# Kernel optimization log

Measured on AMD Instinct MI355X. Metric: run time of the kernel, lower is better.

The kernel has to match this reference:

```python
import jax, jax.numpy as jnp
import numpy as np

N = 100000      # nodes
E = 3200000     # edges (avg degree 32)
F_IN = 512
HID = 256
CLS = 64


def _linear_init(k, fan_in, fan_out):
    lim = 1.0 / np.sqrt(fan_in)
    kw, kb = jax.random.split(k)
    W = jax.random.uniform(kw, (fan_in, fan_out), jnp.float32, -lim, lim)
    b = jax.random.uniform(kb, (fan_out,), jnp.float32, -lim, lim)
    return W, b


def setup_inputs() -> dict:
    key = jax.random.key(0)
    ks = jax.random.split(key, 8)
    x = jax.random.normal(ks[0], (N, F_IN), jnp.float32)
    edge_src = jax.random.randint(ks[1], (E,), 0, N, jnp.int32)
    off = jax.random.randint(ks[2], (E,), 1, N, jnp.int32)
    edge_dst = ((edge_src + off) % N).astype(jnp.int32)  # no self loops
    Wm0, bm0 = _linear_init(ks[3], F_IN, HID)
    Wv0, bv0 = _linear_init(ks[4], F_IN, HID)
    Wm1, bm1 = _linear_init(ks[5], HID, CLS)
    Wv1, bv1 = _linear_init(ks[6], HID, CLS)
    sample = jax.random.normal(ks[7], (N, CLS), jnp.float32)
    return dict(x=x, Wm0=Wm0, bm0=bm0, Wv0=Wv0, bv0=bv0,
                Wm1=Wm1, bm1=bm1, Wv1=Wv1, bv1=bv1,
                sample=sample, edge_src=edge_src, edge_dst=edge_dst)


def reference(x, Wm0, bm0, Wv0, bv0, Wm1, bm1, Wv1, bv1, sample, edge_src, edge_dst):
    n = x.shape[0]
    loops = jnp.arange(n, dtype=edge_src.dtype)
    src = jnp.concatenate([edge_src, loops])  # fill_diag(adj, 1.0)
    dst = jnp.concatenate([edge_dst, loops])
    ones = jnp.ones(src.shape[0], x.dtype)
    deg = jax.ops.segment_sum(ones, src, num_segments=n)
    dis = jnp.where(deg > 0, deg ** -0.5, 0.0)   # D^-0.5
    di = jnp.where(deg > 0, 1.0 / deg, 0.0)      # D^-1
    w0 = dis[src] * dis[dst]                      # adj0 = D^-0.5 A D^-0.5
    w1 = di[src] * di[dst]                        # adj1 = D^-1  A D^-1

    def spmm(w, m):  # (adj @ m) with edge weights w
        return jax.ops.segment_sum(w[:, None] * m[dst], src, num_segments=n)

    # layer 0 (initial=True): no aggregation, dropout off (eval)
    mean = jax.nn.elu(x @ Wm0 + bm0)
    var = jax.nn.relu(x @ Wv0 + bv0)
    # layer 1: variance-attention + dual SpMM
    mean = jax.nn.elu(mean @ Wm1 + bm1)
    var = jax.nn.relu(var @ Wv1 + bv1) + 1e-6
    attn = jnp.exp(-var)
    mean = spmm(w0, mean * attn)
    var = spmm(w1, var * attn * attn)

    out = mean + sample * jnp.sqrt(var)
    return jax.nn.log_softmax(out, axis=-1)
```

## Files before the change

### kernel.cpp

```cpp
#include <hip/hip_runtime.h>
#include <cstdint>
#include <cstddef>


typedef _Float16 h8 __attribute__((ext_vector_type(8)));
typedef _Float16 h2 __attribute__((ext_vector_type(2)));
typedef float f32x4 __attribute__((ext_vector_type(4)));
typedef unsigned int uint32;

#define BSHIFT 7
#define NCHUNK 256

static __device__ __forceinline__ float elu_f(float z) {
  return z > 0.f ? z : expm1f(z);
}

static __device__ __forceinline__ void gload16(const void* g, void* l) {
  __builtin_amdgcn_global_load_lds(
      (__attribute__((address_space(1))) void*)g,
      (__attribute__((address_space(3))) void*)l, 16, 0, 0);
}

__global__ __launch_bounds__(256) void hist_k(const int* __restrict__ esrc, int E,
                                              int chunk, int* __restrict__ h, int NB) {
  __shared__ int sh[1024];
  int t = threadIdx.x;
  for (int i = t; i < NB; i += 256) sh[i] = 0;
  __syncthreads();
  int e0 = blockIdx.x * chunk;
  int e1 = min(e0 + chunk, E);
  for (int e = e0 + t; e < e1; e += 256) atomicAdd(&sh[esrc[e] >> BSHIFT], 1);
  __syncthreads();
  for (int i = t; i < NB; i += 256) h[blockIdx.x * NB + i] = sh[i];
}

__global__ __launch_bounds__(256) void btotal_k(const int* __restrict__ h,
                                                int* __restrict__ tot, int NB) {
  int b = blockIdx.x, t = threadIdx.x;
  int v = h[t * NB + b];
#pragma unroll
  for (int off = 32; off; off >>= 1) v += __shfl_xor(v, off, 64);
  __shared__ int sw[4];
  if ((t & 63) == 0) sw[t >> 6] = v;
  __syncthreads();
  if (t == 0) tot[b] = sw[0] + sw[1] + sw[2] + sw[3];
}

__global__ __launch_bounds__(1024) void bscan_k(const int* __restrict__ tot,
                                                int* __restrict__ base, int NB) {
  __shared__ int sh[1024];
  int t = threadIdx.x;
  int v = (t < NB) ? tot[t] : 0;
  sh[t] = v;
  __syncthreads();
  for (int off = 1; off < 1024; off <<= 1) {
    int add = (t >= off) ? sh[t - off] : 0;
    __syncthreads();
    sh[t] += add;
    __syncthreads();
  }
  if (t < NB) base[t] = sh[t] - v;
  if (t == 1023) base[NB] = sh[1023];
}

__global__ __launch_bounds__(256) void boff_k(int* __restrict__ h,
                                              const int* __restrict__ base, int NB) {
  __shared__ int sh[256];
  int b = blockIdx.x, t = threadIdx.x;
  int v = h[t * NB + b];
  sh[t] = v;
  __syncthreads();
  for (int off = 1; off < 256; off <<= 1) {
    int add = (t >= off) ? sh[t - off] : 0;
    __syncthreads();
    sh[t] += add;
    __syncthreads();
  }
  h[t * NB + b] = base[b] + sh[t] - v;
}

__global__ __launch_bounds__(256) void bscatter_k(
    const int* __restrict__ esrc, const int* __restrict__ edst, int E, int chunk,
    const int* __restrict__ h, int2* __restrict__ pairs, int NB) {
  __shared__ int lcur[1024];
  int t = threadIdx.x;
  for (int i = t; i < NB; i += 256) lcur[i] = h[blockIdx.x * NB + i];
  __syncthreads();
  int e0 = blockIdx.x * chunk;
  int e1 = min(e0 + chunk, E);
  for (int e = e0 + t; e < e1; e += 256) {
    int s = esrc[e], d = edst[e];
    int pos = atomicAdd(&lcur[s >> BSHIFT], 1);
    pairs[pos] = make_int2(s, d);
  }
}

__global__ __launch_bounds__(256) void countN_k(
    const int2* __restrict__ pairs, const int* __restrict__ base,
    int* __restrict__ cnt, float2* __restrict__ dd, int n) {
  __shared__ int c128[128];
  int b = blockIdx.x, t = threadIdx.x;
  if (t < 128) c128[t] = 0;
  __syncthreads();
  int lo = base[b], hi = base[b + 1];
  for (int i = lo + t; i < hi; i += 256) atomicAdd(&c128[pairs[i].x & 127], 1);
  __syncthreads();
  if (t < 128) {
    int node = b * 128 + t;
    if (node < n) {
      int c = c128[t];
      cnt[node] = c;
      float d = (float)(c + 1);
      dd[node] = make_float2(rsqrtf(d), 1.f / d);
    }
  }
}

__global__ __launch_bounds__(256) void partC_k(
    const int2* __restrict__ pairs, const int* __restrict__ base,
    const int* __restrict__ rs, int* __restrict__ csr, int n) {
  __shared__ int lcur[128];
  int b = blockIdx.x, t = threadIdx.x;
  if (t < 128) {
    int node = b * 128 + t;
    lcur[t] = (node < n) ? rs[node] : 0;
  }
  __syncthreads();
  int lo = base[b], hi = base[b + 1];
  for (int i = lo + t; i < hi; i += 256) {
    int2 pr = pairs[i];
    int pos = atomicAdd(&lcur[pr.x & 127], 1);
    csr[pos] = pr.y;
  }
}

__global__ void scan1_k(const int* __restrict__ cnt, int* __restrict__ excl,
                        int* __restrict__ bsum, int n) {
  __shared__ int sh[256];
  int t = threadIdx.x, idx = blockIdx.x * 256 + t;
  int v = (idx < n) ? ((cnt[idx] + 3) & ~3) : 0;
  sh[t] = v;
  __syncthreads();
  for (int off = 1; off < 256; off <<= 1) {
    int add = (t >= off) ? sh[t - off] : 0;
    __syncthreads();
    sh[t] += add;
    __syncthreads();
  }
  if (idx < n) excl[idx] = sh[t] - v;
  if (t == 255) bsum[blockIdx.x] = sh[255];
}

__global__ void scan2_k(const int* __restrict__ bsum, int* __restrict__ boff, int nb) {
  __shared__ int sh[512];
  int t = threadIdx.x;
  int v = (t < nb) ? bsum[t] : 0;
  sh[t] = v;
  __syncthreads();
  for (int off = 1; off < 512; off <<= 1) {
    int add = (t >= off) ? sh[t - off] : 0;
    __syncthreads();
    sh[t] += add;
    __syncthreads();
  }
  if (t < nb) boff[t] = sh[t] - v;
}

__global__ void scan3_k(int* __restrict__ excl, const int* __restrict__ boff, int n) {
  int idx = blockIdx.x * 256 + threadIdx.x;
  if (idx < n) excl[idx] += boff[blockIdx.x];
}

__global__ void prep_w_k(const float* __restrict__ Wm0, const float* __restrict__ Wv0,
                         const float* __restrict__ Wm1, const float* __restrict__ Wv1,
                         _Float16* __restrict__ W1t, _Float16* __restrict__ W2t) {
  int idx = blockIdx.x * 256 + threadIdx.x;
  if (idx < 512 * 512) {
    int n = idx >> 9, k = idx & 511;
    float v = (n < 256) ? Wm0[k * 256 + n] : Wv0[k * 256 + (n - 256)];
    W1t[idx] = (_Float16)v;
  }
  if (idx < 128 * 512) {
    int n = idx >> 9, k = idx & 511;
    float v = 0.f;
    if (n < 64) { if (k < 256) v = Wm1[k * 64 + n]; }
    else        { if (k >= 256) v = Wv1[(k - 256) * 64 + (n - 64)]; }
    W2t[idx] = (_Float16)v;
  }
}

__global__ __launch_bounds__(512, 2) void gemm1_k(
    const float* __restrict__ A, const _Float16* __restrict__ Bt,
    const float* __restrict__ b0, const float* __restrict__ b1,
    _Float16* __restrict__ out, int M) {
  __shared__ __align__(16) unsigned char ldsb[98304];

  const int m0 = blockIdx.x * 128;
  const int t = threadIdx.x;
  const int lane = t & 63;
  const int wave = t >> 6;
  const int wm = wave >> 2;
  const int wn = wave & 3;
  const int lr = lane & 15, quad = lane >> 4;

  const int ra = t >> 3;
  const int sa = t & 7;
  const int asw = (sa ^ (ra & 7)) << 2;
  const int rb = t >> 2;
  const int sb = t & 3;
  const int bsw = (sb ^ (rb & 3)) << 3;

  f32x4 acc[4][8] = {};

  auto stage = [&](int b, int kt) {
#pragma unroll
    for (int i = 0; i < 2; i++) {
      int r = i * 64 + ra;
      const float* src = A + (size_t)min(m0 + r, M - 1) * 512 + kt + asw;
      gload16(src, ldsb + b * 16384 + i * 8192 + t * 16);
    }
#pragma unroll
    for (int i = 0; i < 4; i++) {
      int r = i * 128 + rb;
      const _Float16* src = Bt + (size_t)r * 512 + kt + bsw;
      gload16(src, ldsb + 32768 + b * 32768 + i * 8192 + t * 16);
    }
  };

  stage(0, 0);
  __syncthreads();

  int cur = 0;
  const int zA = lr & 7;
  const int zB = lr & 3;
  for (int kt = 0; kt < 512; kt += 32) {
    if (kt + 32 < 512) stage(cur ^ 1, kt + 32);
    const unsigned char* Ab = ldsb + cur * 16384;
    const unsigned char* Bb = ldsb + 32768 + cur * 32768;
    h8 bf[8];
#pragma unroll
    for (int j = 0; j < 8; j++) {
      int row = wn * 128 + j * 16 + lr;
      bf[j] = *(const h8*)(Bb + row * 64 + ((quad ^ zB) << 4));
    }
#pragma unroll
    for (int i = 0; i < 4; i++) {
      int R = wm * 64 + i * 16 + lr;
      const float4 a0 = *(const float4*)(Ab + R * 128 + (((2 * quad) ^ zA) << 4));
      const float4 a1 = *(const float4*)(Ab + R * 128 + (((2 * quad + 1) ^ zA) << 4));
      h8 af = {(_Float16)a0.x, (_Float16)a0.y, (_Float16)a0.z, (_Float16)a0.w,
               (_Float16)a1.x, (_Float16)a1.y, (_Float16)a1.z, (_Float16)a1.w};
#pragma unroll
      for (int j = 0; j < 8; j++)
        acc[i][j] = __builtin_amdgcn_mfma_f32_16x16x32_f16(af, bf[j], acc[i][j], 0, 0, 0);
    }
    __syncthreads();
    cur ^= 1;
  }

  _Float16* lt = (_Float16*)ldsb;
  for (int hh = 0; hh < 2; hh++) {
    if (wm == hh) {
#pragma unroll
      for (int j = 0; j < 8; j++) {
        int col = wn * 128 + j * 16 + lr;
        float bj = (col < 256) ? b0[col] : b1[col - 256];
#pragma unroll
        for (int i = 0; i < 4; i++) {
#pragma unroll
          for (int r = 0; r < 4; r++) {
            float z = acc[i][j][r] + bj;
            float v = (col < 256) ? elu_f(z) : fmaxf(z, 0.f);
            lt[(i * 16 + quad * 4 + r) * 520 + col] = (_Float16)v;
          }
        }
      }
    }
    __syncthreads();
    {
      int row = t >> 3;
      int gr = m0 + hh * 64 + row;
      if (gr < M) {
        _Float16* dst = out + (size_t)gr * 512;
        const _Float16* srow = lt + row * 520;
#pragma unroll
        for (int k = 0; k < 8; k++) {
          int c0 = ((t & 7) + k * 8) * 8;
          *(h8*)(dst + c0) = *(const h8*)(srow + c0);
        }
      }
    }
    __syncthreads();
  }
}

__global__ __launch_bounds__(256) void gemm2_k(
    const _Float16* __restrict__ A, const _Float16* __restrict__ Bt,
    const float* __restrict__ bm1, const float* __restrict__ bv1,
    uint32* __restrict__ Mcat, int M, int K) {
  __shared__ _Float16 lds[20480];
  _Float16* As = lds;
  _Float16* Bs = lds + 10240;
  const int m0 = blockIdx.x * 128;
  const int t = threadIdx.x;
  const int lane = t & 63;
  const int wave = t >> 6;
  const int lr = lane & 15, quad = lane >> 4;
  const int trow = t >> 2;
  const int tkc = (t & 3) * 8;

  const size_t arow0 = (size_t)min(m0 + trow, M - 1) * K;
  const size_t arow1 = (size_t)min(m0 + trow + 64, M - 1) * K;
  const size_t brow0 = (size_t)trow * K;
  const size_t brow1 = (size_t)(trow + 64) * K;

  f32x4 acc[2][8] = {};
  h8 pa[2], pb[2];

  pa[0] = *(const h8*)(A + arow0 + tkc);
  pa[1] = *(const h8*)(A + arow1 + tkc);
  pb[0] = *(const h8*)(Bt + brow0 + tkc);
  pb[1] = *(const h8*)(Bt + brow1 + tkc);
  *(h8*)&As[trow * 40 + tkc] = pa[0];
  *(h8*)&As[(trow + 64) * 40 + tkc] = pa[1];
  *(h8*)&Bs[trow * 40 + tkc] = pb[0];
  *(h8*)&Bs[(trow + 64) * 40 + tkc] = pb[1];
  __syncthreads();

  for (int kt = 0; kt < K; kt += 32) {
    const int cur = (kt >> 5) & 1;
    const int curo = cur * 5120;
    const bool more = (kt + 32) < K;
    if (more) {
      pa[0] = *(const h8*)(A + arow0 + kt + 32 + tkc);
      pa[1] = *(const h8*)(A + arow1 + kt + 32 + tkc);
      pb[0] = *(const h8*)(Bt + brow0 + kt + 32 + tkc);
      pb[1] = *(const h8*)(Bt + brow1 + kt + 32 + tkc);
    }
    h8 af[2], bf[8];
#pragma unroll
    for (int i = 0; i < 2; i++)
      af[i] = *(h8*)&As[curo + (wave * 32 + i * 16 + lr) * 40 + quad * 8];
#pragma unroll
    for (int j = 0; j < 8; j++)
      bf[j] = *(h8*)&Bs[curo + (j * 16 + lr) * 40 + quad * 8];
#pragma unroll
    for (int i = 0; i < 2; i++)
#pragma unroll
      for (int j = 0; j < 8; j++)
        acc[i][j] = __builtin_amdgcn_mfma_f32_16x16x32_f16(af[i], bf[j], acc[i][j], 0, 0, 0);
    if (more) {
      const int nxto = (cur ^ 1) * 5120;
      *(h8*)&As[nxto + trow * 40 + tkc] = pa[0];
      *(h8*)&As[nxto + (trow + 64) * 40 + tkc] = pa[1];
      *(h8*)&Bs[nxto + trow * 40 + tkc] = pb[0];
      *(h8*)&Bs[nxto + (trow + 64) * 40 + tkc] = pb[1];
      __syncthreads();
    }
  }

#pragma unroll
  for (int jm = 0; jm < 4; jm++) {
    int c = jm * 16 + lr;
    float bm = bm1[c], bv = bv1[c];
#pragma unroll
    for (int i = 0; i < 2; i++) {
#pragma unroll
      for (int r = 0; r < 4; r++) {
        int gr = m0 + wave * 32 + i * 16 + quad * 4 + r;
        if (gr < M) {
          float zm = acc[i][jm][r] + bm;
          float zv = acc[i][4 + jm][r] + bv;
          float m = elu_f(zm);
          float v = fmaxf(zv, 0.f) + 1e-6f;
          float a = __expf(-v);
          h2 pk;
          pk.x = (_Float16)(m * a);
          pk.y = (_Float16)(v * a * a);
          Mcat[(size_t)gr * 64 + c] = __builtin_bit_cast(uint32, pk);
        }
      }
    }
  }
}

__global__ __launch_bounds__(256) void spmm_final_k(
    const uint32* __restrict__ Mcat, const float2* __restrict__ dd,
    const int* __restrict__ row_start, const int* __restrict__ cnt,
    const int* __restrict__ csr, const float* __restrict__ sample,
    float* __restrict__ out, int n) {
  int wid = threadIdx.x >> 6, lane = threadIdx.x & 63;
  int r = blockIdx.x * 4 + wid;
  if (r >= n) return;
  float2 wr = dd[r];
  h2 self = __builtin_bit_cast(h2, Mcat[(size_t)r * 64 + lane]);
  float Sm = wr.x * (float)self.x;
  float Sv = wr.y * (float)self.y;
  int start = __builtin_amdgcn_readfirstlane(row_start[r]);
  int c = __builtin_amdgcn_readfirstlane(cnt[r]);
  int j = 0;
  for (; j + 4 <= c; j += 4) {
    int4 d4 = *(const int4*)(csr + start + j);
    float2 w0 = dd[d4.x];
    float2 w1 = dd[d4.y];
    float2 w2 = dd[d4.z];
    float2 w3 = dd[d4.w];
    h2 p0 = __builtin_bit_cast(h2, Mcat[(size_t)d4.x * 64 + lane]);
    h2 p1 = __builtin_bit_cast(h2, Mcat[(size_t)d4.y * 64 + lane]);
    h2 p2 = __builtin_bit_cast(h2, Mcat[(size_t)d4.z * 64 + lane]);
    h2 p3 = __builtin_bit_cast(h2, Mcat[(size_t)d4.w * 64 + lane]);
    Sm += w0.x * (float)p0.x; Sv += w0.y * (float)p0.y;
    Sm += w1.x * (float)p1.x; Sv += w1.y * (float)p1.y;
    Sm += w2.x * (float)p2.x; Sv += w2.y * (float)p2.y;
    Sm += w3.x * (float)p3.x; Sv += w3.y * (float)p3.y;
  }
  for (; j < c; j++) {
    int d = csr[start + j];
    float2 w = dd[d];
    h2 p = __builtin_bit_cast(h2, Mcat[(size_t)d * 64 + lane]);
    Sm += w.x * (float)p.x;
    Sv += w.y * (float)p.y;
  }
  float mean = wr.x * Sm;
  float var = wr.y * Sv;
  float o = mean + sample[(size_t)r * 64 + lane] * sqrtf(var);
  float mx = o;
#pragma unroll
  for (int off = 32; off; off >>= 1) mx = fmaxf(mx, __shfl_xor(mx, off, 64));
  float ex = __expf(o - mx);
  float s = ex;
#pragma unroll
  for (int off = 32; off; off >>= 1) s += __shfl_xor(s, off, 64);
  out[(size_t)r * 64 + lane] = o - mx - logf(s);
}

extern "C" void kernel_launch(void* const* d_in, const int* in_sizes, int n_in,
                              void* d_out, int out_size, void* d_ws, size_t ws_size,
                              hipStream_t stream) {
  (void)n_in; (void)out_size; (void)ws_size;
  const float* x    = (const float*)d_in[0];
  const float* Wm0  = (const float*)d_in[1];
  const float* bm0  = (const float*)d_in[2];
  const float* Wv0  = (const float*)d_in[3];
  const float* bv0  = (const float*)d_in[4];
  const float* Wm1  = (const float*)d_in[5];
  const float* bm1  = (const float*)d_in[6];
  const float* Wv1  = (const float*)d_in[7];
  const float* bv1  = (const float*)d_in[8];
  const float* sample = (const float*)d_in[9];
  const int* esrc   = (const int*)d_in[10];
  const int* edst   = (const int*)d_in[11];
  float* out = (float*)d_out;

  const int N = in_sizes[0] / 512;
  const int E = in_sizes[10];
  const int NB = (N + 127) >> BSHIFT;
  const int chunk = (E + NCHUNK - 1) / NCHUNK;

  uint8_t* p = (uint8_t*)d_ws;
  size_t off = 0;
  auto alloc = [&](size_t bytes) -> void* {
    void* r = p + off;
    off += (bytes + 255) & ~(size_t)255;
    return r;
  };
  _Float16* W1t  = (_Float16*)alloc((size_t)512 * 512 * 2);
  _Float16* W2t  = (_Float16*)alloc((size_t)128 * 512 * 2);
  _Float16* Hcat = (_Float16*)alloc((size_t)N * 512 * 2);
  uint32*   Mcat = (uint32*)alloc((size_t)N * 64 * 4);
  int*   cnt    = (int*)alloc((size_t)N * 4);
  float2* dd    = (float2*)alloc((size_t)N * 8);
  int*   rs     = (int*)alloc((size_t)N * 4);
  int*   h      = (int*)alloc((size_t)NCHUNK * NB * 4);
  int*   tot    = (int*)alloc((size_t)(NB + 1) * 4);
  int*   base   = (int*)alloc((size_t)(NB + 1) * 4);
  int*   bsum   = (int*)alloc(2048);
  int*   boff   = (int*)alloc(2048);
  int*   csr    = (int*)alloc((size_t)(E + 4 * N) * 4);
  int2* pairs = (int2*)Hcat;

  const int nbN = (N + 255) / 256;

  prep_w_k<<<(512 * 512 + 255) / 256, 256, 0, stream>>>(Wm0, Wv0, Wm1, Wv1, W1t, W2t);
  hist_k<<<NCHUNK, 256, 0, stream>>>(esrc, E, chunk, h, NB);
  btotal_k<<<NB, 256, 0, stream>>>(h, tot, NB);
  bscan_k<<<1, 1024, 0, stream>>>(tot, base, NB);
  boff_k<<<NB, 256, 0, stream>>>(h, base, NB);
  bscatter_k<<<NCHUNK, 256, 0, stream>>>(esrc, edst, E, chunk, h, pairs, NB);
  countN_k<<<NB, 256, 0, stream>>>(pairs, base, cnt, dd, N);
  scan1_k<<<nbN, 256, 0, stream>>>(cnt, rs, bsum, N);
  scan2_k<<<1, 512, 0, stream>>>(bsum, boff, nbN);
  scan3_k<<<nbN, 256, 0, stream>>>(rs, boff, N);
  partC_k<<<NB, 256, 0, stream>>>(pairs, base, rs, csr, N);

  const int mtiles = (N + 127) / 128;
  gemm1_k<<<mtiles, 512, 0, stream>>>(x, W1t, bm0, bv0, Hcat, N);
  gemm2_k<<<mtiles, 256, 0, stream>>>(Hcat, W2t, bm1, bv1, Mcat, N, 512);
  spmm_final_k<<<(N + 3) / 4, 256, 0, stream>>>(Mcat, dd, rs, cnt, csr, sample, out, N);
}
```

Before: 796.8 us.

## Retile gemm1 to 128x128 output tiles with grouped N-tile scheduling

Result: faster. 720.8 us (-9.5%).

```diff
diff --git a/kernel.cpp b/kernel.cpp
--- a/kernel.cpp
+++ b/kernel.cpp
@@ -189,41 +189,40 @@
   }
 }
 
-__global__ __launch_bounds__(512, 2) void gemm1_k(
+__global__ __launch_bounds__(256) void gemm1_k(
     const float* __restrict__ A, const _Float16* __restrict__ Bt,
     const float* __restrict__ b0, const float* __restrict__ b1,
-    _Float16* __restrict__ out, int M) {
-  __shared__ __align__(16) unsigned char ldsb[98304];
-
-  const int m0 = blockIdx.x * 128;
+    _Float16* __restrict__ out, int M, int mtiles) {
+  __shared__ __align__(16) unsigned char ldsb[49152];
+
+  const int sg = blockIdx.x >> 5, loc = blockIdx.x & 31;
+  const int nt = loc >> 3, mtl = loc & 7;
+  const int mt = sg * 8 + mtl;
+  if (mt >= mtiles) return;
+  const int m0 = mt * 128, n0 = nt * 128;
   const int t = threadIdx.x;
   const int lane = t & 63;
   const int wave = t >> 6;
-  const int wm = wave >> 2;
-  const int wn = wave & 3;
+  const int wm = wave >> 1, wn = wave & 1;
   const int lr = lane & 15, quad = lane >> 4;
 
   const int ra = t >> 3;
-  const int sa = t & 7;
-  const int asw = (sa ^ (ra & 7)) << 2;
+  const int asw = ((t & 7) ^ (ra & 7)) << 2;
   const int rb = t >> 2;
-  const int sb = t & 3;
-  const int bsw = (sb ^ (rb & 3)) << 3;
-
-  f32x4 acc[4][8] = {};
+  const int bsw = ((t & 3) ^ ((t >> 3) & 3)) << 3;
+
+  f32x4 acc[4][4] = {};
 
   auto stage = [&](int b, int kt) {
 #pragma unroll
+    for (int i = 0; i < 4; i++) {
+      const float* src = A + (size_t)min(m0 + i * 32 + ra, M - 1) * 512 + kt + asw;
+      gload16(src, ldsb + b * 16384 + i * 4096 + t * 16);
+    }
+#pragma unroll
     for (int i = 0; i < 2; i++) {
-      int r = i * 64 + ra;
-      const float* src = A + (size_t)min(m0 + r, M - 1) * 512 + kt + asw;
-      gload16(src, ldsb + b * 16384 + i * 8192 + t * 16);
-    }
-#pragma unroll
-    for (int i = 0; i < 4; i++) {
-      int r = i * 128 + rb;
-      const _Float16* src = Bt + (size_t)r * 512 + kt + bsw;
-      gload16(src, ldsb + 32768 + b * 32768 + i * 8192 + t * 16);
+      const _Float16* src = Bt + (size_t)(n0 + i * 64 + rb) * 512 + kt + bsw;
+      gload16(src, ldsb + 32768 + b * 8192 + i * 4096 + t * 16);
     }
   };
 
@@ -232,65 +231,60 @@
 
   int cur = 0;
   const int zA = lr & 7;
-  const int zB = lr & 3;
+  const int zB = (lr >> 1) & 3;
   for (int kt = 0; kt < 512; kt += 32) {
     if (kt + 32 < 512) stage(cur ^ 1, kt + 32);
     const unsigned char* Ab = ldsb + cur * 16384;
-    const unsigned char* Bb = ldsb + 32768 + cur * 32768;
-    h8 bf[8];
-#pragma unroll
-    for (int j = 0; j < 8; j++) {
-      int row = wn * 128 + j * 16 + lr;
+    const unsigned char* Bb = ldsb + 32768 + cur * 8192;
+    h8 bf[4];
+#pragma unroll
+    for (int j = 0; j < 4; j++) {
+      int row = wn * 64 + j * 16 + lr;
       bf[j] = *(const h8*)(Bb + row * 64 + ((quad ^ zB) << 4));
     }
+    h8 af[4];
 #pragma unroll
     for (int i = 0; i < 4; i++) {
       int R = wm * 64 + i * 16 + lr;
       const float4 a0 = *(const float4*)(Ab + R * 128 + (((2 * quad) ^ zA) << 4));
       const float4 a1 = *(const float4*)(Ab + R * 128 + (((2 * quad + 1) ^ zA) << 4));
-      h8 af = {(_Float16)a0.x, (_Float16)a0.y, (_Float16)a0.z, (_Float16)a0.w,
-               (_Float16)a1.x, (_Float16)a1.y, (_Float16)a1.z, (_Float16)a1.w};
-#pragma unroll
-      for (int j = 0; j < 8; j++)
-        acc[i][j] = __builtin_amdgcn_mfma_f32_16x16x32_f16(af, bf[j], acc[i][j], 0, 0, 0);
-    }
+      af[i] = h8{(_Float16)a0.x, (_Float16)a0.y, (_Float16)a0.z, (_Float16)a0.w,
+                 (_Float16)a1.x, (_Float16)a1.y, (_Float16)a1.z, (_Float16)a1.w};
+    }
+#pragma unroll
+    for (int i = 0; i < 4; i++)
+#pragma unroll
+      for (int j = 0; j < 4; j++)
+        acc[i][j] = __builtin_amdgcn_mfma_f32_16x16x32_f16(af[i], bf[j], acc[i][j], 0, 0, 0);
     __syncthreads();
     cur ^= 1;
   }
 
   _Float16* lt = (_Float16*)ldsb;
-  for (int hh = 0; hh < 2; hh++) {
-    if (wm == hh) {
-#pragma unroll
-      for (int j = 0; j < 8; j++) {
-        int col = wn * 128 + j * 16 + lr;
-        float bj = (col < 256) ? b0[col] : b1[col - 256];
-#pragma unroll
-        for (int i = 0; i < 4; i++) {
-#pragma unroll
-          for (int r = 0; r < 4; r++) {
-            float z = acc[i][j][r] + bj;
-            float v = (col < 256) ? elu_f(z) : fmaxf(z, 0.f);
-            lt[(i * 16 + quad * 4 + r) * 520 + col] = (_Float16)v;
-          }
-        }
+#pragma unroll
+  for (int j = 0; j < 4; j++) {
+    int gc = n0 + wn * 64 + j * 16 + lr;
+    float bj = (gc < 256) ? b0[gc] : b1[gc - 256];
+#pragma unroll
+    for (int i = 0; i < 4; i++) {
+#pragma unroll
+      for (int r = 0; r < 4; r++) {
+        float z = acc[i][j][r] + bj;
+        float v = (gc < 256) ? elu_f(z) : fmaxf(z, 0.f);
+        lt[(wm * 64 + i * 16 + quad * 4 + r) * 136 + wn * 64 + j * 16 + lr] = (_Float16)v;
       }
     }
-    __syncthreads();
-    {
-      int row = t >> 3;
-      int gr = m0 + hh * 64 + row;
-      if (gr < M) {
-        _Float16* dst = out + (size_t)gr * 512;
-        const _Float16* srow = lt + row * 520;
-#pragma unroll
-        for (int k = 0; k < 8; k++) {
-          int c0 = ((t & 7) + k * 8) * 8;
-          *(h8*)(dst + c0) = *(const h8*)(srow + c0);
-        }
-      }
-    }
-    __syncthreads();
+  }
+  __syncthreads();
+  {
+    const int row = t >> 1, col0 = (t & 1) * 64;
+    const int gr = m0 + row;
+    if (gr < M) {
+      _Float16* dst = out + (size_t)gr * 512 + n0 + col0;
+#pragma unroll
+      for (int k = 0; k < 8; k++)
+        *(h8*)(dst + k * 8) = *(h8*)&lt[row * 136 + col0 + k * 8];
+    }
   }
 }
 
@@ -494,7 +488,8 @@
   partC_k<<<NB, 256, 0, stream>>>(pairs, base, rs, csr, N);
 
   const int mtiles = (N + 127) / 128;
-  gemm1_k<<<mtiles, 512, 0, stream>>>(x, W1t, bm0, bv0, Hcat, N);
+  const int sgroups = (mtiles + 7) / 8;
+  gemm1_k<<<sgroups * 32, 256, 0, stream>>>(x, W1t, bm0, bv0, Hcat, N, mtiles);
   gemm2_k<<<mtiles, 256, 0, stream>>>(Hcat, W2t, bm1, bv1, Mcat, N, 512);
   spmm_final_k<<<(N + 3) / 4, 256, 0, stream>>>(Mcat, dd, rs, cnt, csr, sample, out, N);
 }
```
